# Performance work log

Measured on AMD Instinct MI355X. Metric: run time of the kernel, lower is better.

The kernel has to match this reference:

```python
import jax, jax.numpy as jnp
import numpy as np

N_NODES = 50000
N_EDGES = 800000
IN_CH, HID_CH, OUT_CH = 128, 128, 64


def setup_inputs() -> dict:
    key = jax.random.key(0)
    k1, k2, k3, k4, k5, k6 = jax.random.split(key, 6)
    x = jax.random.normal(k1, (N_NODES, IN_CH), dtype=jnp.float32)
    edge_index = jax.random.randint(k2, (2, N_EDGES), 0, N_NODES, dtype=jnp.int64)
    # nn.Linear params: W [out, in], b [out]
    W1 = jax.random.normal(k3, (HID_CH, IN_CH), dtype=jnp.float32) / np.sqrt(IN_CH)
    b1 = jax.random.normal(k4, (HID_CH,), dtype=jnp.float32) * 0.01
    W2 = jax.random.normal(k5, (OUT_CH, HID_CH), dtype=jnp.float32) / np.sqrt(HID_CH)
    b2 = jax.random.normal(k6, (OUT_CH,), dtype=jnp.float32) * 0.01
    return {"x": x, "edge_index": edge_index, "W1": W1, "b1": b1, "W2": W2, "b2": b2}


def _aggregate(x, edge_index):
    # Faithful to SimpleGNN.aggregate: deg from ROW counts, normalization gathered at DST (col).
    row, col = edge_index[0], edge_index[1]
    n = x.shape[0]
    deg = jnp.bincount(row, length=n).astype(x.dtype)
    deg_inv = jnp.where(deg > 0, 1.0 / deg, 0.0)
    # out[dst] += x[src] * deg_inv[dst]  ==  segment_sum(x[src] by dst) * deg_inv[dst]
    agg = jax.ops.segment_sum(x[row], col, num_segments=n)
    return agg * deg_inv[:, None]


def reference(x, edge_index, W1, b1, W2, b2):
    h = x @ W1.T + b1                 # [N, hidden]
    h = _aggregate(h, edge_index)     # degree-normalized scatter-add
    out = h @ W2.T + b2               # [N, out]
    return out
```

## Files before the change

### kernel.cpp

```cpp
#include <hip/hip_runtime.h>
#include <hip/hip_bf16.h>


#define IN_CH   128
#define OUT_CH  64
#define NCHUNK  64
#define NRANGE  8
#define RBINS   6272
#define NRANGE_H 4
#define RBINS_H 12544
#define MC_PAD  40
#define YROWS   32
#define PLACE_BLOCKS (NCHUNK * NRANGE)
#define SMEM_FLOATS (IN_CH * OUT_CH + YROWS * (IN_CH + 4))

typedef unsigned short u16;
typedef unsigned int u32;

static __device__ inline float bfu32_lo(u32 u) { return __uint_as_float(u << 16); }
static __device__ inline float bfu32_hi(u32 u) { return __uint_as_float(u & 0xffff0000u); }
static __device__ inline u16 f2bf(float f) {
    __hip_bfloat16 h = __float2bfloat16(f);
    return *reinterpret_cast<u16*>(&h);
}

static __device__ inline int detect_stride_wave(const int* __restrict__ ei) {
    int lane = threadIdx.x & 63;
    int idx = (lane < 32) ? (2 * lane + 1) : 1;
    int v = ei[idx];
    unsigned long long m = __ballot((v != 0) && (lane < 32));
    return (m == 0ull) ? 2 : 1;
}

static __device__ inline void y_unit(int t, const float* __restrict__ x,
                                     const float* __restrict__ M,
                                     u16* __restrict__ y, float* smem,
                                     int n_nodes) {
    int tid = threadIdx.x;
    float* Ms = smem;
    float (*xs)[IN_CH + 4] = (float(*)[IN_CH + 4])(smem + IN_CH * OUT_CH);
    int tx = tid & 15;
    int ty = tid >> 4;
    int row0 = t * YROWS;
    if (row0 >= n_nodes) return;

    const float4* Mv = (const float4*)M;
    float4* Msv = (float4*)Ms;
#pragma unroll
    for (int k = 0; k < 8; ++k) Msv[tid + 256 * k] = Mv[tid + 256 * k];

    for (int f = tid; f < YROWS * 32; f += 256) {
        int r = f >> 5, kq = f & 31;
        float4 v = make_float4(0.f, 0.f, 0.f, 0.f);
        if (row0 + r < n_nodes)
            v = *(const float4*)&x[(size_t)(row0 + r) * IN_CH + 4 * kq];
        *(float4*)&xs[r][4 * kq] = v;
    }
    __syncthreads();

    float4 acc0 = make_float4(0.f, 0.f, 0.f, 0.f);
    float4 acc1 = make_float4(0.f, 0.f, 0.f, 0.f);

    for (int k = 0; k < IN_CH; k += 4) {
        float4 xr0 = *(const float4*)&xs[ty][k];
        float4 xr1 = *(const float4*)&xs[ty + 16][k];
        float4 m0 = *(const float4*)&Ms[(k + 0) * OUT_CH + 4 * tx];
        float4 m1 = *(const float4*)&Ms[(k + 1) * OUT_CH + 4 * tx];
        float4 m2 = *(const float4*)&Ms[(k + 2) * OUT_CH + 4 * tx];
        float4 m3 = *(const float4*)&Ms[(k + 3) * OUT_CH + 4 * tx];
        acc0.x = fmaf(xr0.x, m0.x, acc0.x); acc0.y = fmaf(xr0.x, m0.y, acc0.y);
        acc0.z = fmaf(xr0.x, m0.z, acc0.z); acc0.w = fmaf(xr0.x, m0.w, acc0.w);
        acc0.x = fmaf(xr0.y, m1.x, acc0.x); acc0.y = fmaf(xr0.y, m1.y, acc0.y);
        acc0.z = fmaf(xr0.y, m1.z, acc0.z); acc0.w = fmaf(xr0.y, m1.w, acc0.w);
        acc0.x = fmaf(xr0.z, m2.x, acc0.x); acc0.y = fmaf(xr0.z, m2.y, acc0.y);
        acc0.z = fmaf(xr0.z, m2.z, acc0.z); acc0.w = fmaf(xr0.z, m2.w, acc0.w);
        acc0.x = fmaf(xr0.w, m3.x, acc0.x); acc0.y = fmaf(xr0.w, m3.y, acc0.y);
        acc0.z = fmaf(xr0.w, m3.z, acc0.z); acc0.w = fmaf(xr0.w, m3.w, acc0.w);
        acc1.x = fmaf(xr1.x, m0.x, acc1.x); acc1.y = fmaf(xr1.x, m0.y, acc1.y);
        acc1.z = fmaf(xr1.x, m0.z, acc1.z); acc1.w = fmaf(xr1.x, m0.w, acc1.w);
        acc1.x = fmaf(xr1.y, m1.x, acc1.x); acc1.y = fmaf(xr1.y, m1.y, acc1.y);
        acc1.z = fmaf(xr1.y, m1.z, acc1.z); acc1.w = fmaf(xr1.y, m1.w, acc1.w);
        acc1.x = fmaf(xr1.z, m2.x, acc1.x); acc1.y = fmaf(xr1.z, m2.y, acc1.y);
        acc1.z = fmaf(xr1.z, m2.z, acc1.z); acc1.w = fmaf(xr1.z, m2.w, acc1.w);
        acc1.x = fmaf(xr1.w, m3.x, acc1.x); acc1.y = fmaf(xr1.w, m3.y, acc1.y);
        acc1.z = fmaf(xr1.w, m3.z, acc1.z); acc1.w = fmaf(xr1.w, m3.w, acc1.w);
    }

    int r0 = row0 + ty;
    int r1 = row0 + ty + 16;
    if (r0 < n_nodes) {
        ushort4 s4;
        s4.x = f2bf(acc0.x); s4.y = f2bf(acc0.y);
        s4.z = f2bf(acc0.z); s4.w = f2bf(acc0.w);
        *(ushort4*)&y[(size_t)r0 * OUT_CH + 4 * tx] = s4;
    }
    if (r1 < n_nodes) {
        ushort4 s4;
        s4.x = f2bf(acc1.x); s4.y = f2bf(acc1.y);
        s4.z = f2bf(acc1.z); s4.w = f2bf(acc1.w);
        *(ushort4*)&y[(size_t)r1 * OUT_CH + 4 * tx] = s4;
    }
}

__global__ __launch_bounds__(256) void mk_prep(const float* __restrict__ W1,
                                               const float* __restrict__ b1,
                                               const float* __restrict__ W2,
                                               const int* __restrict__ ei,
                                               float* __restrict__ M,
                                               float* __restrict__ c,
                                               u16* __restrict__ row_slab,
                                               u16* __restrict__ col_slab,
                                               int* __restrict__ counter,
                                               int n_edges, int n_nodes) {
    __shared__ u32 bins[RBINS_H];
    int b = blockIdx.x;
    int tid = threadIdx.x;
    if (b < MC_PAD) {
        if (b == 0 && tid == 0) *counter = 0;
        int t = b * 256 + tid;
        if (t < IN_CH * OUT_CH) {
            int o = t & (OUT_CH - 1);
            int i = t >> 6;
            float acc = 0.f;
            for (int h = 0; h < 128; ++h)
                acc += W1[h * 128 + i] * W2[o * 128 + h];
            M[i * OUT_CH + o] = acc;
        } else if (t < IN_CH * OUT_CH + OUT_CH) {
            int o = t - IN_CH * OUT_CH;
            float acc = 0.f;
            for (int h = 0; h < 128; ++h)
                acc += b1[h] * W2[o * 128 + h];
            c[o] = acc;
        }
        return;
    }
    int hb = b - MC_PAD;
    int range = hb & (NRANGE_H - 1);
    int chunk = hb >> 2;

    int range_size = (n_nodes + NRANGE_H - 1) / NRANGE_H;
    int lo = range * range_size;
    int hi = lo + range_size; if (hi > n_nodes) hi = n_nodes;
    int nbins = hi - lo;
    if (nbins <= 0) return;

    int stride = detect_stride_wave(ei);
    for (int i = tid; i < nbins; i += 256) bins[i] = 0u;
    __syncthreads();

    size_t e0 = (size_t)chunk * n_edges / NCHUNK;
    size_t e1 = (size_t)(chunk + 1) * n_edges / NCHUNK;
    size_t cnt = e1 - e0;
    const int* rp = ei;
    const int* cp = ei + (size_t)n_edges * stride;

    size_t i = tid;
    int s[8], d[8];
    for (; i + 1792 < cnt; i += 2048) {
#pragma unroll
        for (int k = 0; k < 8; ++k) s[k] = rp[(e0 + i + 256 * k) * stride];
#pragma unroll
        for (int k = 0; k < 8; ++k) d[k] = cp[(e0 + i + 256 * k) * stride];
#pragma unroll
        for (int k = 0; k < 8; ++k) {
            if (s[k] >= lo && s[k] < hi) atomicAdd(&bins[s[k] - lo], 1u);
            if (d[k] >= lo && d[k] < hi && (unsigned)s[k] < (unsigned)n_nodes)
                atomicAdd(&bins[d[k] - lo], 0x10000u);
        }
    }
    for (; i < cnt; i += 256) {
        int ss = rp[(e0 + i) * stride];
        int dd = cp[(e0 + i) * stride];
        if (ss >= lo && ss < hi) atomicAdd(&bins[ss - lo], 1u);
        if (dd >= lo && dd < hi && (unsigned)ss < (unsigned)n_nodes)
            atomicAdd(&bins[dd - lo], 0x10000u);
    }
    __syncthreads();

    size_t base = (size_t)chunk * n_nodes + lo;
    for (int k = tid; k < nbins; k += 256) {
        u32 v = bins[k];
        row_slab[base + k] = (u16)(v & 0xFFFFu);
        col_slab[base + k] = (u16)(v >> 16);
    }
}

__global__ __launch_bounds__(256) void mk_choff_y(u16* __restrict__ row_slab,
                                                  u16* __restrict__ col_slab,
                                                  int* __restrict__ deg_row,
                                                  int* __restrict__ cnt_col,
                                                  int* __restrict__ cursor_part,
                                                  int* __restrict__ bsums,
                                                  int* __restrict__ counter,
                                                  int* __restrict__ bscan_g,
                                                  const float* __restrict__ x,
                                                  const float* __restrict__ M,
                                                  u16* __restrict__ y,
                                                  int n_nodes, int nb) {
    __shared__ float smem[SMEM_FLOATS];
    __shared__ int islast;
    int b = blockIdx.x;
    int t = threadIdx.x;

    if (b >= nb) {
        y_unit(b - nb, x, M, y, smem, n_nodes);
        return;
    }

    int* sm = (int*)smem;
    int n = b * 256 + t;
    int run = 0;
    if (n < n_nodes) {
        int sum = 0;
#pragma unroll 8
        for (int ch = 0; ch < NCHUNK; ++ch)
            sum += row_slab[(size_t)ch * n_nodes + n];
        deg_row[n] = sum;
#pragma unroll 8
        for (int ch = 0; ch < NCHUNK; ++ch) {
            int v = col_slab[(size_t)ch * n_nodes + n];
            col_slab[(size_t)ch * n_nodes + n] = (u16)run;
            run += v;
        }
        cnt_col[n] = run;
    }
    sm[t] = run;
    __syncthreads();
    for (int d = 1; d < 256; d <<= 1) {
        int add = (t >= d) ? sm[t - d] : 0;
        __syncthreads();
        sm[t] += add;
        __syncthreads();
    }
    if (n < n_nodes) cursor_part[n] = sm[t] - run;
    if (t == 255) bsums[b] = sm[t];

    __syncthreads();
    if (t == 0) {
        __threadfence();
        int old = atomicAdd(counter, 1);
        islast = (old == nb - 1);
    }
    __syncthreads();
    if (islast) {
        int v = (t < nb) ? atomicAdd(&bsums[t], 0) : 0;
        sm[t] = v;
        __syncthreads();
        for (int d = 1; d < 256; d <<= 1) {
            int add = (t >= d) ? sm[t - d] : 0;
            __syncthreads();
            sm[t] += add;
            __syncthreads();
        }
        bscan_g[t] = sm[t] - v;
    }
}

__global__ __launch_bounds__(256) void mk_place_y(const int* __restrict__ ei,
                                                  const int* __restrict__ cursor_part,
                                                  const int* __restrict__ bscan_g,
                                                  const u16* __restrict__ col_slab,
                                                  int* __restrict__ csr_src,
                                                  const float* __restrict__ x,
                                                  const float* __restrict__ M,
                                                  u16* __restrict__ y,
                                                  int n_edges, int n_nodes,
                                                  int y_split) {
    __shared__ float smem[SMEM_FLOATS];
    int b = blockIdx.x;
    int tid = threadIdx.x;

    if (b < PLACE_BLOCKS) {
        int* rank = (int*)smem;
        int* bscanL = (int*)smem + RBINS;

        int range = b & (NRANGE - 1);
        int chunk = b >> 3;
        int range_size = (n_nodes + NRANGE - 1) / NRANGE;
        int lo = range * range_size;
        int hi = lo + range_size; if (hi > n_nodes) hi = n_nodes;
        if (hi <= lo) return;

        int stride = detect_stride_wave(ei);
        bscanL[tid] = bscan_g[tid];
        for (int i = tid; i < hi - lo; i += 256) rank[i] = 0;
        __syncthreads();

        size_t e0 = (size_t)chunk * n_edges / NCHUNK;
        size_t e1 = (size_t)(chunk + 1) * n_edges / NCHUNK;
        size_t cnt = e1 - e0;
        const int* rp = ei;
        const int* cp = ei + (size_t)n_edges * stride;
        size_t slab_base = (size_t)chunk * n_nodes;

        size_t i = tid;
        int s[8], d[8], cpart[8], coff[8];
        for (; i + 1792 < cnt; i += 2048) {
#pragma unroll
            for (int k = 0; k < 8; ++k) s[k] = rp[(e0 + i + 256 * k) * stride];
#pragma unroll
            for (int k = 0; k < 8; ++k) d[k] = cp[(e0 + i + 256 * k) * stride];
#pragma unroll
            for (int k = 0; k < 8; ++k) {
                int dc = (d[k] >= lo && d[k] < hi) ? d[k] : lo;
                cpart[k] = cursor_part[dc];
                coff[k]  = (int)col_slab[slab_base + dc];
            }
#pragma unroll
            for (int k = 0; k < 8; ++k) {
                if (d[k] >= lo && d[k] < hi && (unsigned)s[k] < (unsigned)n_nodes) {
                    int r = atomicAdd(&rank[d[k] - lo], 1);
                    csr_src[cpart[k] + bscanL[d[k] >> 8] + coff[k] + r] = s[k];
                }
            }
        }
        for (; i < cnt; i += 256) {
            int ss = rp[(e0 + i) * stride];
            int dd = cp[(e0 + i) * stride];
            if (dd >= lo && dd < hi && (unsigned)ss < (unsigned)n_nodes) {
                int r = atomicAdd(&rank[dd - lo], 1);
                csr_src[cursor_part[dd] + bscanL[dd >> 8] + (int)col_slab[slab_base + dd] + r] = ss;
            }
        }
        return;
    }

    y_unit(y_split + (b - PLACE_BLOCKS), x, M, y, smem, n_nodes);
}

__global__ __launch_bounds__(256) void mk_agg_final(const int* __restrict__ cursor_part,
                                                    const int* __restrict__ bscan_g,
                                                    const int* __restrict__ cnt_col,
                                                    const int* __restrict__ csr_src,
                                                    const int* __restrict__ deg_row,
                                                    const uint2* __restrict__ yv,
                                                    const float* __restrict__ c,
                                                    const float* __restrict__ b2,
                                                    float* __restrict__ out,
                                                    int n_nodes) {
    int wave = threadIdx.x >> 6;
    int lane = threadIdx.x & 63;
    int dsub = lane >> 4;
    int ch   = lane & 15;
    int d = blockIdx.x * 16 + wave * 4 + dsub;
    if (d >= n_nodes) return;

    int start = cursor_part[d] + bscan_g[d >> 8];
    int cnt = cnt_col[d];
    int end = start + cnt;
    int e1m = end - 1;
    float a0 = 0.f, a1 = 0.f, a2 = 0.f, a3 = 0.f;
    for (int j = start; j < end; j += 8) {
        int idx[8], srcs[8];
#pragma unroll
        for (int k = 0; k < 8; ++k) {
            int t = j + k;
            idx[k] = t > e1m ? e1m : t;
        }
#pragma unroll
        for (int k = 0; k < 8; ++k) srcs[k] = csr_src[idx[k]];
        uint2 u[8];
#pragma unroll
        for (int k = 0; k < 8; ++k) u[k] = yv[(size_t)srcs[k] * 16 + ch];
#pragma unroll
        for (int k = 1; k < 8; ++k)
            if (j + k >= end) { u[k].x = 0u; u[k].y = 0u; }
#pragma unroll
        for (int k = 0; k < 8; ++k) {
            a0 += bfu32_lo(u[k].x);
            a1 += bfu32_hi(u[k].x);
            a2 += bfu32_lo(u[k].y);
            a3 += bfu32_hi(u[k].y);
        }
    }
    int dr = deg_row[d];
    float di = (dr > 0) ? (1.0f / (float)dr) : 0.f;
    float fc = di * (float)cnt;
    float4 cv = ((const float4*)c)[ch];
    float4 bv = ((const float4*)b2)[ch];
    float4 o;
    o.x = di * a0 + fc * cv.x + bv.x;
    o.y = di * a1 + fc * cv.y + bv.y;
    o.z = di * a2 + fc * cv.z + bv.z;
    o.w = di * a3 + fc * cv.w + bv.w;
    ((float4*)(out + (size_t)d * OUT_CH))[ch] = o;
}

extern "C" void kernel_launch(void* const* d_in, const int* in_sizes, int n_in,
                              void* d_out, int out_size, void* d_ws, size_t ws_size,
                              hipStream_t stream) {
    const float* x  = (const float*)d_in[0];
    const int*   ei = (const int*)d_in[1];
    const float* W1 = (const float*)d_in[2];
    const float* b1 = (const float*)d_in[3];
    const float* W2 = (const float*)d_in[4];
    const float* b2 = (const float*)d_in[5];
    float* out = (float*)d_out;

    const int n_nodes = in_sizes[0] / IN_CH;
    const int n_edges = in_sizes[1] / 2;

    const size_t slab_bytes = (((size_t)NCHUNK * n_nodes * 2) + 127) & ~(size_t)127;
    const size_t csr_bytes  = ((size_t)n_edges * 4 + 127) & ~(size_t)127;

    char* ws = (char*)d_ws;
    float* M        = (float*)(ws);
    float* c        = (float*)(ws + 32768);
    int*   deg_row  = (int*)  (ws + 33152);
    int*   cnt_col  = (int*)  (ws + 233216);
    int*   cursor   = (int*)  (ws + 433280);
    int*   bsums    = (int*)  (ws + 633344);
    int*   bscan_g  = (int*)  (ws + 634368);
    int*   counter  = (int*)  (ws + 635392);
    u16*   row_slab = (u16*)  (ws + 635520);
    u16*   col_slab = (u16*)  (ws + 635520 + slab_bytes);
    int*   csr_src  = (int*)  (ws + 635520 + 2 * slab_bytes);
    u16*   y        = (u16*)  (ws + 635520 + 2 * slab_bytes + csr_bytes);

    const int y_total = (n_nodes + YROWS - 1) / YROWS;
    const int nb = (n_nodes + 255) / 256;
    int y_split = 512 - nb;
    if (y_split > y_total) y_split = y_total;

    mk_prep<<<MC_PAD + NCHUNK * NRANGE_H, 256, 0, stream>>>(
        W1, b1, W2, ei, M, c, row_slab, col_slab, counter, n_edges, n_nodes);

    mk_choff_y<<<nb + y_split, 256, 0, stream>>>(
        row_slab, col_slab, deg_row, cnt_col, cursor, bsums, counter, bscan_g,
        x, M, y, n_nodes, nb);

    mk_place_y<<<PLACE_BLOCKS + (y_total - y_split), 256, 0, stream>>>(
        ei, cursor, bscan_g, col_slab, csr_src, x, M, y, n_edges, n_nodes,
        y_split);

    mk_agg_final<<<(n_nodes + 15) / 16, 256, 0, stream>>>(
        cursor, bscan_g, cnt_col, csr_src, deg_row, (const uint2*)y, c, b2, out,
        n_nodes);
}
```

Before: 156.1 us.

## Record per-edge rank during histogram to make CSR placement atomic-free

The histogram pass now stores, for each edge, the per-chunk rank returned by the shared-memory atomic on its destination bin. The placement kernel reads that rank instead of redoing shared atomics over node ranges, so each edge is read once rather than once per range, and the work splits into 256 sub-chunk blocks. The y-projection work moves entirely into the placement kernel, the choff kernel shrinks to scan work only, and chunk/range block indexing is reordered. The cost is an extra u16 per edge written and read through global memory.

```diff
diff --git a/kernel.cpp b/kernel.cpp
--- a/kernel.cpp
+++ b/kernel.cpp
@@ -5,13 +5,11 @@
 #define IN_CH   128
 #define OUT_CH  64
 #define NCHUNK  64
-#define NRANGE  8
-#define RBINS   6272
 #define NRANGE_H 4
 #define RBINS_H 12544
 #define MC_PAD  40
 #define YROWS   32
-#define PLACE_BLOCKS (NCHUNK * NRANGE)
+#define PLACE_BLOCKS 256
 #define SMEM_FLOATS (IN_CH * OUT_CH + YROWS * (IN_CH + 4))
 
 typedef unsigned short u16;
@@ -110,6 +108,7 @@
                                                float* __restrict__ c,
                                                u16* __restrict__ row_slab,
                                                u16* __restrict__ col_slab,
+                                               u16* __restrict__ erank,
                                                int* __restrict__ counter,
                                                int n_edges, int n_nodes) {
     __shared__ u32 bins[RBINS_H];
@@ -135,8 +134,8 @@
         return;
     }
     int hb = b - MC_PAD;
-    int range = hb & (NRANGE_H - 1);
-    int chunk = hb >> 2;
+    int chunk = hb & (NCHUNK - 1);
+    int range = hb >> 6;
 
     int range_size = (n_nodes + NRANGE_H - 1) / NRANGE_H;
     int lo = range * range_size;
@@ -164,16 +163,20 @@
 #pragma unroll
         for (int k = 0; k < 8; ++k) {
             if (s[k] >= lo && s[k] < hi) atomicAdd(&bins[s[k] - lo], 1u);
-            if (d[k] >= lo && d[k] < hi && (unsigned)s[k] < (unsigned)n_nodes)
-                atomicAdd(&bins[d[k] - lo], 0x10000u);
+            if (d[k] >= lo && d[k] < hi && (unsigned)s[k] < (unsigned)n_nodes) {
+                u32 old = atomicAdd(&bins[d[k] - lo], 0x10000u);
+                erank[e0 + i + 256 * k] = (u16)(old >> 16);
+            }
         }
     }
     for (; i < cnt; i += 256) {
         int ss = rp[(e0 + i) * stride];
         int dd = cp[(e0 + i) * stride];
         if (ss >= lo && ss < hi) atomicAdd(&bins[ss - lo], 1u);
-        if (dd >= lo && dd < hi && (unsigned)ss < (unsigned)n_nodes)
-            atomicAdd(&bins[dd - lo], 0x10000u);
+        if (dd >= lo && dd < hi && (unsigned)ss < (unsigned)n_nodes) {
+            u32 old = atomicAdd(&bins[dd - lo], 0x10000u);
+            erank[e0 + i] = (u16)(old >> 16);
+        }
     }
     __syncthreads();
 
@@ -185,29 +188,19 @@
     }
 }
 
-__global__ __launch_bounds__(256) void mk_choff_y(u16* __restrict__ row_slab,
-                                                  u16* __restrict__ col_slab,
-                                                  int* __restrict__ deg_row,
-                                                  int* __restrict__ cnt_col,
-                                                  int* __restrict__ cursor_part,
-                                                  int* __restrict__ bsums,
-                                                  int* __restrict__ counter,
-                                                  int* __restrict__ bscan_g,
-                                                  const float* __restrict__ x,
-                                                  const float* __restrict__ M,
-                                                  u16* __restrict__ y,
-                                                  int n_nodes, int nb) {
-    __shared__ float smem[SMEM_FLOATS];
+__global__ __launch_bounds__(256) void mk_choff(u16* __restrict__ row_slab,
+                                                u16* __restrict__ col_slab,
+                                                int* __restrict__ deg_row,
+                                                int* __restrict__ cnt_col,
+                                                int* __restrict__ cursor_part,
+                                                int* __restrict__ bsums,
+                                                int* __restrict__ counter,
+                                                int* __restrict__ bscan_g,
+                                                int n_nodes, int nb) {
+    __shared__ int sm[256];
     __shared__ int islast;
     int b = blockIdx.x;
     int t = threadIdx.x;
-
-    if (b >= nb) {
-        y_unit(b - nb, x, M, y, smem, n_nodes);
-        return;
-    }
-
-    int* sm = (int*)smem;
     int n = b * 256 + t;
     int run = 0;
     if (n < n_nodes) {
@@ -260,72 +253,70 @@
                                                   const int* __restrict__ cursor_part,
                                                   const int* __restrict__ bscan_g,
                                                   const u16* __restrict__ col_slab,
+                                                  const u16* __restrict__ erank,
                                                   int* __restrict__ csr_src,
                                                   const float* __restrict__ x,
                                                   const float* __restrict__ M,
                                                   u16* __restrict__ y,
-                                                  int n_edges, int n_nodes,
-                                                  int y_split) {
+                                                  int n_edges, int n_nodes) {
     __shared__ float smem[SMEM_FLOATS];
     int b = blockIdx.x;
     int tid = threadIdx.x;
 
     if (b < PLACE_BLOCKS) {
-        int* rank = (int*)smem;
-        int* bscanL = (int*)smem + RBINS;
-
-        int range = b & (NRANGE - 1);
-        int chunk = b >> 3;
-        int range_size = (n_nodes + NRANGE - 1) / NRANGE;
-        int lo = range * range_size;
-        int hi = lo + range_size; if (hi > n_nodes) hi = n_nodes;
-        if (hi <= lo) return;
-
+        int* bscanL = (int*)smem;
+        bscanL[tid] = bscan_g[tid];
+        __syncthreads();
+
+        int chunk = b >> 2;
+        int sub = b & 3;
         int stride = detect_stride_wave(ei);
-        bscanL[tid] = bscan_g[tid];
-        for (int i = tid; i < hi - lo; i += 256) rank[i] = 0;
-        __syncthreads();
 
         size_t e0 = (size_t)chunk * n_edges / NCHUNK;
         size_t e1 = (size_t)(chunk + 1) * n_edges / NCHUNK;
         size_t cnt = e1 - e0;
+        size_t s0 = e0 + (size_t)sub * cnt / 4;
+        size_t s1 = e0 + (size_t)(sub + 1) * cnt / 4;
         const int* rp = ei;
         const int* cp = ei + (size_t)n_edges * stride;
         size_t slab_base = (size_t)chunk * n_nodes;
 
-        size_t i = tid;
-        int s[8], d[8], cpart[8], coff[8];
-        for (; i + 1792 < cnt; i += 2048) {
-#pragma unroll
-            for (int k = 0; k < 8; ++k) s[k] = rp[(e0 + i + 256 * k) * stride];
-#pragma unroll
-            for (int k = 0; k < 8; ++k) d[k] = cp[(e0 + i + 256 * k) * stride];
-#pragma unroll
-            for (int k = 0; k < 8; ++k) {
-                int dc = (d[k] >= lo && d[k] < hi) ? d[k] : lo;
+        size_t i = s0 + tid;
+        int s4[4], d4[4], cpart[4], coff[4];
+        u16 r4[4];
+        for (; i + 768 < s1; i += 1024) {
+#pragma unroll
+            for (int k = 0; k < 4; ++k) s4[k] = rp[(i + 256 * k) * stride];
+#pragma unroll
+            for (int k = 0; k < 4; ++k) d4[k] = cp[(i + 256 * k) * stride];
+#pragma unroll
+            for (int k = 0; k < 4; ++k) r4[k] = erank[i + 256 * k];
+#pragma unroll
+            for (int k = 0; k < 4; ++k) {
+                int dc = ((unsigned)d4[k] < (unsigned)n_nodes) ? d4[k] : 0;
                 cpart[k] = cursor_part[dc];
                 coff[k]  = (int)col_slab[slab_base + dc];
             }
 #pragma unroll
-            for (int k = 0; k < 8; ++k) {
-                if (d[k] >= lo && d[k] < hi && (unsigned)s[k] < (unsigned)n_nodes) {
-                    int r = atomicAdd(&rank[d[k] - lo], 1);
-                    csr_src[cpart[k] + bscanL[d[k] >> 8] + coff[k] + r] = s[k];
+            for (int k = 0; k < 4; ++k) {
+                if ((unsigned)d4[k] < (unsigned)n_nodes &&
+                    (unsigned)s4[k] < (unsigned)n_nodes) {
+                    csr_src[cpart[k] + bscanL[d4[k] >> 8] + coff[k] + (int)r4[k]] = s4[k];
                 }
             }
         }
-        for (; i < cnt; i += 256) {
-            int ss = rp[(e0 + i) * stride];
-            int dd = cp[(e0 + i) * stride];
-            if (dd >= lo && dd < hi && (unsigned)ss < (unsigned)n_nodes) {
-                int r = atomicAdd(&rank[dd - lo], 1);
-                csr_src[cursor_part[dd] + bscanL[dd >> 8] + (int)col_slab[slab_base + dd] + r] = ss;
+        for (; i < s1; i += 256) {
+            int ss = rp[i * stride];
+            int dd = cp[i * stride];
+            if ((unsigned)dd < (unsigned)n_nodes && (unsigned)ss < (unsigned)n_nodes) {
+                csr_src[cursor_part[dd] + bscanL[dd >> 8] +
+                        (int)col_slab[slab_base + dd] + (int)erank[i]] = ss;
             }
         }
         return;
     }
 
-    y_unit(y_split + (b - PLACE_BLOCKS), x, M, y, smem, n_nodes);
+    y_unit(b - PLACE_BLOCKS, x, M, y, smem, n_nodes);
 }
 
 __global__ __launch_bounds__(256) void mk_agg_final(const int* __restrict__ cursor_part,
@@ -402,6 +393,7 @@
 
     const size_t slab_bytes = (((size_t)NCHUNK * n_nodes * 2) + 127) & ~(size_t)127;
     const size_t csr_bytes  = ((size_t)n_edges * 4 + 127) & ~(size_t)127;
+    const size_t y_bytes    = ((size_t)n_nodes * OUT_CH * 2 + 127) & ~(size_t)127;
 
     char* ws = (char*)d_ws;
     float* M        = (float*)(ws);
@@ -416,22 +408,22 @@
     u16*   col_slab = (u16*)  (ws + 635520 + slab_bytes);
     int*   csr_src  = (int*)  (ws + 635520 + 2 * slab_bytes);
     u16*   y        = (u16*)  (ws + 635520 + 2 * slab_bytes + csr_bytes);
+    u16*   erank    = (u16*)  (ws + 635520 + 2 * slab_bytes + csr_bytes + y_bytes);
 
     const int y_total = (n_nodes + YROWS - 1) / YROWS;
     const int nb = (n_nodes + 255) / 256;
-    int y_split = 512 - nb;
-    if (y_split > y_total) y_split = y_total;
 
     mk_prep<<<MC_PAD + NCHUNK * NRANGE_H, 256, 0, stream>>>(
-        W1, b1, W2, ei, M, c, row_slab, col_slab, counter, n_edges, n_nodes);
-
-    mk_choff_y<<<nb + y_split, 256, 0, stream>>>(
-        row_slab, col_slab, deg_row, cnt_col, cursor, bsums, counter, bscan_g,
-        x, M, y, n_nodes, nb);
-
-    mk_place_y<<<PLACE_BLOCKS + (y_total - y_split), 256, 0, stream>>>(
-        ei, cursor, bscan_g, col_slab, csr_src, x, M, y, n_edges, n_nodes,
-        y_split);
+        W1, b1, W2, ei, M, c, row_slab, col_slab, erank, counter,
+        n_edges, n_nodes);
+
+    mk_choff<<<nb, 256, 0, stream>>>(row_slab, col_slab, deg_row, cnt_col,
+                                     cursor, bsums, counter, bscan_g,
+                                     n_nodes, nb);
+
+    mk_place_y<<<PLACE_BLOCKS + y_total, 256, 0, stream>>>(
+        ei, cursor, bscan_g, col_slab, erank, csr_src, x, M, y,
+        n_edges, n_nodes);
 
     mk_agg_final<<<(n_nodes + 15) / 16, 256, 0, stream>>>(
         cursor, bscan_g, cnt_col, csr_src, deg_row, (const uint2*)y, c, b2, out,
```

Result: no change. 158.4 us (+1.5%).

## Merge four launches into two persistent kernels with grid-wide spin barriers

Applied to the files above, without the earlier changes.

Replaces the four-kernel pipeline with a zeroing kernel plus two persistent kernels. Inside each, phases are separated by atomic-counter spin barriers and work is handed out through atomic ticket queues. Phase 1 fuses the weight premultiply, the histogram, and the column offset/scan. Phase 2 fuses CSR placement with the y GEMM units, then aggregation in a grid-stride loop. The goal is to cut launch gaps and tail idling between stages. The risk is that the spin barriers deadlock unless every block is co-resident, and the single launch caps occupancy.

```diff
diff --git a/kernel.cpp b/kernel.cpp
--- a/kernel.cpp
+++ b/kernel.cpp
@@ -9,10 +9,17 @@
 #define RBINS   6272
 #define NRANGE_H 4
 #define RBINS_H 12544
-#define MC_PAD  40
 #define YROWS   32
-#define PLACE_BLOCKS (NCHUNK * NRANGE)
+#define PLACE_UNITS (NCHUNK * NRANGE)
+#define K1_BLOCKS  (NCHUNK * NRANGE_H)
+#define K2_BLOCKS  512
 #define SMEM_FLOATS (IN_CH * OUT_CH + YROWS * (IN_CH + 4))
+
+#define C_HIST_DONE  0
+#define C_CHOFF_TK   1
+#define C_CHOFF_DONE 2
+#define C_TKA        3
+#define C_DONEA      4
 
 typedef unsigned short u16;
 typedef unsigned int u32;
@@ -30,6 +37,10 @@
     int v = ei[idx];
     unsigned long long m = __ballot((v != 0) && (lane < 32));
     return (m == 0ull) ? 2 : 1;
+}
+
+__global__ __launch_bounds__(64) void mk_zero(int* __restrict__ cnt) {
+    if (threadIdx.x < 32) cnt[threadIdx.x] = 0;
 }
 
 static __device__ inline void y_unit(int t, const float* __restrict__ x,
@@ -102,149 +113,133 @@
     }
 }
 
-__global__ __launch_bounds__(256) void mk_prep(const float* __restrict__ W1,
-                                               const float* __restrict__ b1,
-                                               const float* __restrict__ W2,
-                                               const int* __restrict__ ei,
-                                               float* __restrict__ M,
-                                               float* __restrict__ c,
-                                               u16* __restrict__ row_slab,
-                                               u16* __restrict__ col_slab,
-                                               int* __restrict__ counter,
-                                               int n_edges, int n_nodes) {
-    __shared__ u32 bins[RBINS_H];
+__global__ __launch_bounds__(256) void mk_phase1(const float* __restrict__ W1,
+                                                 const float* __restrict__ b1,
+                                                 const float* __restrict__ W2,
+                                                 const int* __restrict__ ei,
+                                                 float* __restrict__ M,
+                                                 float* __restrict__ c,
+                                                 u16* __restrict__ row_slab,
+                                                 u16* __restrict__ col_slab,
+                                                 int* __restrict__ deg_row,
+                                                 int* __restrict__ cnt_col,
+                                                 int* __restrict__ cursor_part,
+                                                 int* __restrict__ bsums,
+                                                 int* __restrict__ bscan_g,
+                                                 int* __restrict__ cnt,
+                                                 int n_edges, int n_nodes, int nb) {
+    __shared__ __align__(16) u32 bins[RBINS_H];
+    __shared__ int tk, lastf;
     int b = blockIdx.x;
     int tid = threadIdx.x;
-    if (b < MC_PAD) {
-        if (b == 0 && tid == 0) *counter = 0;
-        int t = b * 256 + tid;
-        if (t < IN_CH * OUT_CH) {
-            int o = t & (OUT_CH - 1);
-            int i = t >> 6;
-            float acc = 0.f;
-            for (int h = 0; h < 128; ++h)
-                acc += W1[h * 128 + i] * W2[o * 128 + h];
-            M[i * OUT_CH + o] = acc;
-        } else if (t < IN_CH * OUT_CH + OUT_CH) {
-            int o = t - IN_CH * OUT_CH;
-            float acc = 0.f;
-            for (int h = 0; h < 128; ++h)
-                acc += b1[h] * W2[o * 128 + h];
-            c[o] = acc;
-        }
-        return;
-    }
-    int hb = b - MC_PAD;
-    int range = hb & (NRANGE_H - 1);
-    int chunk = hb >> 2;
-
-    int range_size = (n_nodes + NRANGE_H - 1) / NRANGE_H;
-    int lo = range * range_size;
-    int hi = lo + range_size; if (hi > n_nodes) hi = n_nodes;
-    int nbins = hi - lo;
-    if (nbins <= 0) return;
-
-    int stride = detect_stride_wave(ei);
-    for (int i = tid; i < nbins; i += 256) bins[i] = 0u;
-    __syncthreads();
-
-    size_t e0 = (size_t)chunk * n_edges / NCHUNK;
-    size_t e1 = (size_t)(chunk + 1) * n_edges / NCHUNK;
-    size_t cnt = e1 - e0;
-    const int* rp = ei;
-    const int* cp = ei + (size_t)n_edges * stride;
-
-    size_t i = tid;
-    int s[8], d[8];
-    for (; i + 1792 < cnt; i += 2048) {
-#pragma unroll
-        for (int k = 0; k < 8; ++k) s[k] = rp[(e0 + i + 256 * k) * stride];
-#pragma unroll
-        for (int k = 0; k < 8; ++k) d[k] = cp[(e0 + i + 256 * k) * stride];
-#pragma unroll
-        for (int k = 0; k < 8; ++k) {
-            if (s[k] >= lo && s[k] < hi) atomicAdd(&bins[s[k] - lo], 1u);
-            if (d[k] >= lo && d[k] < hi && (unsigned)s[k] < (unsigned)n_nodes)
-                atomicAdd(&bins[d[k] - lo], 0x10000u);
-        }
-    }
-    for (; i < cnt; i += 256) {
-        int ss = rp[(e0 + i) * stride];
-        int dd = cp[(e0 + i) * stride];
-        if (ss >= lo && ss < hi) atomicAdd(&bins[ss - lo], 1u);
-        if (dd >= lo && dd < hi && (unsigned)ss < (unsigned)n_nodes)
-            atomicAdd(&bins[dd - lo], 0x10000u);
-    }
-    __syncthreads();
-
-    size_t base = (size_t)chunk * n_nodes + lo;
-    for (int k = tid; k < nbins; k += 256) {
-        u32 v = bins[k];
-        row_slab[base + k] = (u16)(v & 0xFFFFu);
-        col_slab[base + k] = (u16)(v >> 16);
-    }
-}
-
-__global__ __launch_bounds__(256) void mk_choff_y(u16* __restrict__ row_slab,
-                                                  u16* __restrict__ col_slab,
-                                                  int* __restrict__ deg_row,
-                                                  int* __restrict__ cnt_col,
-                                                  int* __restrict__ cursor_part,
-                                                  int* __restrict__ bsums,
-                                                  int* __restrict__ counter,
-                                                  int* __restrict__ bscan_g,
-                                                  const float* __restrict__ x,
-                                                  const float* __restrict__ M,
-                                                  u16* __restrict__ y,
-                                                  int n_nodes, int nb) {
-    __shared__ float smem[SMEM_FLOATS];
-    __shared__ int islast;
-    int b = blockIdx.x;
-    int t = threadIdx.x;
-
-    if (b >= nb) {
-        y_unit(b - nb, x, M, y, smem, n_nodes);
-        return;
-    }
-
-    int* sm = (int*)smem;
-    int n = b * 256 + t;
-    int run = 0;
-    if (n < n_nodes) {
-        int sum = 0;
+
+    {
+        int t = b * 33 + tid;
+        if (tid < 33 && t < IN_CH * OUT_CH + OUT_CH) {
+            if (t < IN_CH * OUT_CH) {
+                int o = t & (OUT_CH - 1);
+                int i = t >> 6;
+                float acc = 0.f;
 #pragma unroll 8
-        for (int ch = 0; ch < NCHUNK; ++ch)
-            sum += row_slab[(size_t)ch * n_nodes + n];
-        deg_row[n] = sum;
+                for (int h = 0; h < 128; ++h)
+                    acc += W1[h * 128 + i] * W2[o * 128 + h];
+                M[i * OUT_CH + o] = acc;
+            } else {
+                int o = t - IN_CH * OUT_CH;
+                float acc = 0.f;
 #pragma unroll 8
-        for (int ch = 0; ch < NCHUNK; ++ch) {
-            int v = col_slab[(size_t)ch * n_nodes + n];
-            col_slab[(size_t)ch * n_nodes + n] = (u16)run;
-            run += v;
-        }
-        cnt_col[n] = run;
-    }
-    sm[t] = run;
-    __syncthreads();
-    for (int d = 1; d < 256; d <<= 1) {
-        int add = (t >= d) ? sm[t - d] : 0;
-        __syncthreads();
-        sm[t] += add;
-        __syncthreads();
-    }
-    if (n < n_nodes) cursor_part[n] = sm[t] - run;
-    if (t == 255) bsums[b] = sm[t];
-
-    __syncthreads();
-    if (t == 0) {
+                for (int h = 0; h < 128; ++h)
+                    acc += b1[h] * W2[o * 128 + h];
+                c[o] = acc;
+            }
+        }
+    }
+
+    {
+        int range = b & (NRANGE_H - 1);
+        int chunk = b >> 2;
+        int range_size = (n_nodes + NRANGE_H - 1) / NRANGE_H;
+        int lo = range * range_size;
+        int hi = lo + range_size; if (hi > n_nodes) hi = n_nodes;
+        int nbins = hi - lo;
+        if (nbins > 0) {
+            int stride = detect_stride_wave(ei);
+            for (int i = tid; i < nbins; i += 256) bins[i] = 0u;
+            __syncthreads();
+
+            size_t e0 = (size_t)chunk * n_edges / NCHUNK;
+            size_t e1 = (size_t)(chunk + 1) * n_edges / NCHUNK;
+            size_t cnte = e1 - e0;
+            const int* rp = ei;
+            const int* cp = ei + (size_t)n_edges * stride;
+
+            size_t i = tid;
+            int s[8], d[8];
+            for (; i + 1792 < cnte; i += 2048) {
+#pragma unroll
+                for (int k = 0; k < 8; ++k) s[k] = rp[(e0 + i + 256 * k) * stride];
+#pragma unroll
+                for (int k = 0; k < 8; ++k) d[k] = cp[(e0 + i + 256 * k) * stride];
+#pragma unroll
+                for (int k = 0; k < 8; ++k) {
+                    if (s[k] >= lo && s[k] < hi) atomicAdd(&bins[s[k] - lo], 1u);
+                    if (d[k] >= lo && d[k] < hi && (unsigned)s[k] < (unsigned)n_nodes)
+                        atomicAdd(&bins[d[k] - lo], 0x10000u);
+                }
+            }
+            for (; i < cnte; i += 256) {
+                int ss = rp[(e0 + i) * stride];
+                int dd = cp[(e0 + i) * stride];
+                if (ss >= lo && ss < hi) atomicAdd(&bins[ss - lo], 1u);
+                if (dd >= lo && dd < hi && (unsigned)ss < (unsigned)n_nodes)
+                    atomicAdd(&bins[dd - lo], 0x10000u);
+            }
+            __syncthreads();
+
+            size_t base = (size_t)chunk * n_nodes + lo;
+            for (int k = tid; k < nbins; k += 256) {
+                u32 v = bins[k];
+                row_slab[base + k] = (u16)(v & 0xFFFFu);
+                col_slab[base + k] = (u16)(v >> 16);
+            }
+        }
+    }
+
+    __syncthreads();
+    if (tid == 0) {
         __threadfence();
-        int old = atomicAdd(counter, 1);
-        islast = (old == nb - 1);
-    }
-    __syncthreads();
-    if (islast) {
-        int v = (t < nb) ? atomicAdd(&bsums[t], 0) : 0;
-        sm[t] = v;
+        atomicAdd(&cnt[C_HIST_DONE], 1);
+        while (atomicAdd(&cnt[C_HIST_DONE], 0) < K1_BLOCKS)
+            __builtin_amdgcn_s_sleep(2);
+    }
+    __syncthreads();
+    __threadfence();
+
+    int* sm = (int*)bins;
+    for (;;) {
+        __syncthreads();
+        if (tid == 0) tk = atomicAdd(&cnt[C_CHOFF_TK], 1);
+        __syncthreads();
+        if (tk >= nb) break;
+        int cb = tk;
+        int t = tid;
+        int n = cb * 256 + t;
+        int run = 0;
+        if (n < n_nodes) {
+            int sum = 0;
+#pragma unroll 8
+            for (int ch = 0; ch < NCHUNK; ++ch)
+                sum += row_slab[(size_t)ch * n_nodes + n];
+            deg_row[n] = sum;
+#pragma unroll 8
+            for (int ch = 0; ch < NCHUNK; ++ch) {
+                int v = col_slab[(size_t)ch * n_nodes + n];
+                col_slab[(size_t)ch * n_nodes + n] = (u16)run;
+                run += v;
+            }
+            cnt_col[n] = run;
+        }
+        sm[t] = run;
         __syncthreads();
         for (int d = 1; d < 256; d <<= 1) {
             int add = (t >= d) ? sm[t - d] : 0;
@@ -252,138 +247,182 @@
             sm[t] += add;
             __syncthreads();
         }
-        bscan_g[t] = sm[t] - v;
-    }
-}
-
-__global__ __launch_bounds__(256) void mk_place_y(const int* __restrict__ ei,
-                                                  const int* __restrict__ cursor_part,
-                                                  const int* __restrict__ bscan_g,
-                                                  const u16* __restrict__ col_slab,
-                                                  int* __restrict__ csr_src,
-                                                  const float* __restrict__ x,
-                                                  const float* __restrict__ M,
-                                                  u16* __restrict__ y,
-                                                  int n_edges, int n_nodes,
-                                                  int y_split) {
-    __shared__ float smem[SMEM_FLOATS];
-    int b = blockIdx.x;
-    int tid = threadIdx.x;
-
-    if (b < PLACE_BLOCKS) {
-        int* rank = (int*)smem;
-        int* bscanL = (int*)smem + RBINS;
-
-        int range = b & (NRANGE - 1);
-        int chunk = b >> 3;
-        int range_size = (n_nodes + NRANGE - 1) / NRANGE;
-        int lo = range * range_size;
-        int hi = lo + range_size; if (hi > n_nodes) hi = n_nodes;
-        if (hi <= lo) return;
-
-        int stride = detect_stride_wave(ei);
-        bscanL[tid] = bscan_g[tid];
-        for (int i = tid; i < hi - lo; i += 256) rank[i] = 0;
-        __syncthreads();
-
-        size_t e0 = (size_t)chunk * n_edges / NCHUNK;
-        size_t e1 = (size_t)(chunk + 1) * n_edges / NCHUNK;
-        size_t cnt = e1 - e0;
-        const int* rp = ei;
-        const int* cp = ei + (size_t)n_edges * stride;
-        size_t slab_base = (size_t)chunk * n_nodes;
-
-        size_t i = tid;
-        int s[8], d[8], cpart[8], coff[8];
-        for (; i + 1792 < cnt; i += 2048) {
-#pragma unroll
-            for (int k = 0; k < 8; ++k) s[k] = rp[(e0 + i + 256 * k) * stride];
-#pragma unroll
-            for (int k = 0; k < 8; ++k) d[k] = cp[(e0 + i + 256 * k) * stride];
-#pragma unroll
-            for (int k = 0; k < 8; ++k) {
-                int dc = (d[k] >= lo && d[k] < hi) ? d[k] : lo;
-                cpart[k] = cursor_part[dc];
-                coff[k]  = (int)col_slab[slab_base + dc];
-            }
-#pragma unroll
-            for (int k = 0; k < 8; ++k) {
-                if (d[k] >= lo && d[k] < hi && (unsigned)s[k] < (unsigned)n_nodes) {
-                    int r = atomicAdd(&rank[d[k] - lo], 1);
-                    csr_src[cpart[k] + bscanL[d[k] >> 8] + coff[k] + r] = s[k];
-                }
-            }
-        }
-        for (; i < cnt; i += 256) {
-            int ss = rp[(e0 + i) * stride];
-            int dd = cp[(e0 + i) * stride];
-            if (dd >= lo && dd < hi && (unsigned)ss < (unsigned)n_nodes) {
-                int r = atomicAdd(&rank[dd - lo], 1);
-                csr_src[cursor_part[dd] + bscanL[dd >> 8] + (int)col_slab[slab_base + dd] + r] = ss;
-            }
-        }
-        return;
-    }
-
-    y_unit(y_split + (b - PLACE_BLOCKS), x, M, y, smem, n_nodes);
-}
-
-__global__ __launch_bounds__(256) void mk_agg_final(const int* __restrict__ cursor_part,
+        if (n < n_nodes) cursor_part[n] = sm[t] - run;
+        if (t == 255) bsums[cb] = sm[t];
+
+        __syncthreads();
+        if (t == 0) {
+            __threadfence();
+            int od = atomicAdd(&cnt[C_CHOFF_DONE], 1);
+            lastf = (od == nb - 1);
+        }
+        __syncthreads();
+        if (lastf) {
+            int v = (t < nb) ? atomicAdd(&bsums[t], 0) : 0;
+            sm[t] = v;
+            __syncthreads();
+            for (int d = 1; d < 256; d <<= 1) {
+                int add = (t >= d) ? sm[t - d] : 0;
+                __syncthreads();
+                sm[t] += add;
+                __syncthreads();
+            }
+            bscan_g[t] = sm[t] - v;
+        }
+    }
+}
+
+__global__ __launch_bounds__(256, 2) void mk_phase2(const int* __restrict__ ei,
+                                                    const int* __restrict__ cursor_part,
                                                     const int* __restrict__ bscan_g,
+                                                    const u16* __restrict__ col_slab,
+                                                    int* __restrict__ csr_src,
+                                                    const float* __restrict__ x,
+                                                    const float* __restrict__ M,
+                                                    u16* __restrict__ y,
                                                     const int* __restrict__ cnt_col,
-                                                    const int* __restrict__ csr_src,
                                                     const int* __restrict__ deg_row,
-                                                    const uint2* __restrict__ yv,
                                                     const float* __restrict__ c,
                                                     const float* __restrict__ b2,
                                                     float* __restrict__ out,
-                                                    int n_nodes) {
-    int wave = threadIdx.x >> 6;
-    int lane = threadIdx.x & 63;
+                                                    int* __restrict__ cnt,
+                                                    int n_edges, int n_nodes,
+                                                    int y_total) {
+    __shared__ float smem[SMEM_FLOATS];
+    __shared__ int tk;
+    int tid = threadIdx.x;
+    int totalA = PLACE_UNITS + y_total;
+    int myn = 0;
+
+    for (;;) {
+        __syncthreads();
+        if (tid == 0) tk = atomicAdd(&cnt[C_TKA], 1);
+        __syncthreads();
+        int u = tk;
+        if (u >= totalA) break;
+        if (u < PLACE_UNITS) {
+            int* rank = (int*)smem;
+            int* bscanL = (int*)smem + RBINS;
+
+            int range = u & (NRANGE - 1);
+            int chunk = u >> 3;
+            int range_size = (n_nodes + NRANGE - 1) / NRANGE;
+            int lo = range * range_size;
+            int hi = lo + range_size; if (hi > n_nodes) hi = n_nodes;
+            if (hi > lo) {
+                int stride = detect_stride_wave(ei);
+                bscanL[tid] = bscan_g[tid];
+                for (int i = tid; i < hi - lo; i += 256) rank[i] = 0;
+                __syncthreads();
+
+                size_t e0 = (size_t)chunk * n_edges / NCHUNK;
+                size_t e1 = (size_t)(chunk + 1) * n_edges / NCHUNK;
+                size_t cnte = e1 - e0;
+                const int* rp = ei;
+                const int* cp = ei + (size_t)n_edges * stride;
+                size_t slab_base = (size_t)chunk * n_nodes;
+
+                size_t i = tid;
+                int s[8], d[8], cpart[8], coff[8];
+                for (; i + 1792 < cnte; i += 2048) {
+#pragma unroll
+                    for (int k = 0; k < 8; ++k) s[k] = rp[(e0 + i + 256 * k) * stride];
+#pragma unroll
+                    for (int k = 0; k < 8; ++k) d[k] = cp[(e0 + i + 256 * k) * stride];
+#pragma unroll
+                    for (int k = 0; k < 8; ++k) {
+                        int dc = (d[k] >= lo && d[k] < hi) ? d[k] : lo;
+                        cpart[k] = cursor_part[dc];
+                        coff[k]  = (int)col_slab[slab_base + dc];
+                    }
+#pragma unroll
+                    for (int k = 0; k < 8; ++k) {
+                        if (d[k] >= lo && d[k] < hi && (unsigned)s[k] < (unsigned)n_nodes) {
+                            int r = atomicAdd(&rank[d[k] - lo], 1);
+                            csr_src[cpart[k] + bscanL[d[k] >> 8] + coff[k] + r] = s[k];
+                        }
+                    }
+                }
+                for (; i < cnte; i += 256) {
+                    int ss = rp[(e0 + i) * stride];
+                    int dd = cp[(e0 + i) * stride];
+                    if (dd >= lo && dd < hi && (unsigned)ss < (unsigned)n_nodes) {
+                        int r = atomicAdd(&rank[dd - lo], 1);
+                        csr_src[cursor_part[dd] + bscanL[dd >> 8] +
+                                (int)col_slab[slab_base + dd] + r] = ss;
+                    }
+                }
+            }
+        } else {
+            y_unit(u - PLACE_UNITS, x, M, y, smem, n_nodes);
+        }
+        ++myn;
+    }
+
+    __syncthreads();
+    if (tid == 0) {
+        __threadfence();
+        atomicAdd(&cnt[C_DONEA], myn);
+        while (atomicAdd(&cnt[C_DONEA], 0) < totalA)
+            __builtin_amdgcn_s_sleep(2);
+    }
+    __syncthreads();
+    __threadfence();
+
+    int* bscanL = (int*)smem;
+    bscanL[tid] = bscan_g[tid];
+    __syncthreads();
+
+    int totalB = (n_nodes + 15) / 16;
+    const uint2* yv = (const uint2*)y;
+    int wave = tid >> 6;
+    int lane = tid & 63;
     int dsub = lane >> 4;
     int ch   = lane & 15;
-    int d = blockIdx.x * 16 + wave * 4 + dsub;
-    if (d >= n_nodes) return;
-
-    int start = cursor_part[d] + bscan_g[d >> 8];
-    int cnt = cnt_col[d];
-    int end = start + cnt;
-    int e1m = end - 1;
-    float a0 = 0.f, a1 = 0.f, a2 = 0.f, a3 = 0.f;
-    for (int j = start; j < end; j += 8) {
-        int idx[8], srcs[8];
-#pragma unroll
-        for (int k = 0; k < 8; ++k) {
-            int t = j + k;
-            idx[k] = t > e1m ? e1m : t;
-        }
-#pragma unroll
-        for (int k = 0; k < 8; ++k) srcs[k] = csr_src[idx[k]];
-        uint2 u[8];
-#pragma unroll
-        for (int k = 0; k < 8; ++k) u[k] = yv[(size_t)srcs[k] * 16 + ch];
-#pragma unroll
-        for (int k = 1; k < 8; ++k)
-            if (j + k >= end) { u[k].x = 0u; u[k].y = 0u; }
-#pragma unroll
-        for (int k = 0; k < 8; ++k) {
-            a0 += bfu32_lo(u[k].x);
-            a1 += bfu32_hi(u[k].x);
-            a2 += bfu32_lo(u[k].y);
-            a3 += bfu32_hi(u[k].y);
-        }
-    }
-    int dr = deg_row[d];
-    float di = (dr > 0) ? (1.0f / (float)dr) : 0.f;
-    float fc = di * (float)cnt;
-    float4 cv = ((const float4*)c)[ch];
-    float4 bv = ((const float4*)b2)[ch];
-    float4 o;
-    o.x = di * a0 + fc * cv.x + bv.x;
-    o.y = di * a1 + fc * cv.y + bv.y;
-    o.z = di * a2 + fc * cv.z + bv.z;
-    o.w = di * a3 + fc * cv.w + bv.w;
-    ((float4*)(out + (size_t)d * OUT_CH))[ch] = o;
+    for (int u = blockIdx.x; u < totalB; u += K2_BLOCKS) {
+        int d = u * 16 + wave * 4 + dsub;
+        if (d >= n_nodes) continue;
+
+        int start = cursor_part[d] + bscanL[d >> 8];
+        int cc = cnt_col[d];
+        int end = start + cc;
+        int e1m = end - 1;
+        float a0 = 0.f, a1 = 0.f, a2 = 0.f, a3 = 0.f;
+        for (int j = start; j < end; j += 8) {
+            int idx[8], srcs[8];
+#pragma unroll
+            for (int k = 0; k < 8; ++k) {
+                int t = j + k;
+                idx[k] = t > e1m ? e1m : t;
+            }
+#pragma unroll
+            for (int k = 0; k < 8; ++k) srcs[k] = csr_src[idx[k]];
+            uint2 u8[8];
+#pragma unroll
+            for (int k = 0; k < 8; ++k) u8[k] = yv[(size_t)srcs[k] * 16 + ch];
+#pragma unroll
+            for (int k = 1; k < 8; ++k)
+                if (j + k >= end) { u8[k].x = 0u; u8[k].y = 0u; }
+#pragma unroll
+            for (int k = 0; k < 8; ++k) {
+                a0 += bfu32_lo(u8[k].x);
+                a1 += bfu32_hi(u8[k].x);
+                a2 += bfu32_lo(u8[k].y);
+                a3 += bfu32_hi(u8[k].y);
+            }
+        }
+        int dr = deg_row[d];
+        float di = (dr > 0) ? (1.0f / (float)dr) : 0.f;
+        float fc = di * (float)cc;
+        float4 cv = ((const float4*)c)[ch];
+        float4 bv = ((const float4*)b2)[ch];
+        float4 o;
+        o.x = di * a0 + fc * cv.x + bv.x;
+        o.y = di * a1 + fc * cv.y + bv.y;
+        o.z = di * a2 + fc * cv.z + bv.z;
+        o.w = di * a3 + fc * cv.w + bv.w;
+        ((float4*)(out + (size_t)d * OUT_CH))[ch] = o;
+    }
 }
 
 extern "C" void kernel_launch(void* const* d_in, const int* in_sizes, int n_in,
@@ -411,7 +450,7 @@
     int*   cursor   = (int*)  (ws + 433280);
     int*   bsums    = (int*)  (ws + 633344);
     int*   bscan_g  = (int*)  (ws + 634368);
-    int*   counter  = (int*)  (ws + 635392);
+    int*   counters = (int*)  (ws + 635392);
     u16*   row_slab = (u16*)  (ws + 635520);
     u16*   col_slab = (u16*)  (ws + 635520 + slab_bytes);
     int*   csr_src  = (int*)  (ws + 635520 + 2 * slab_bytes);
@@ -419,21 +458,14 @@
 
     const int y_total = (n_nodes + YROWS - 1) / YROWS;
     const int nb = (n_nodes + 255) / 256;
-    int y_split = 512 - nb;
-    if (y_split > y_total) y_split = y_total;
-
-    mk_prep<<<MC_PAD + NCHUNK * NRANGE_H, 256, 0, stream>>>(
-        W1, b1, W2, ei, M, c, row_slab, col_slab, counter, n_edges, n_nodes);
-
-    mk_choff_y<<<nb + y_split, 256, 0, stream>>>(
-        row_slab, col_slab, deg_row, cnt_col, cursor, bsums, counter, bscan_g,
-        x, M, y, n_nodes, nb);
-
-    mk_place_y<<<PLACE_BLOCKS + (y_total - y_split), 256, 0, stream>>>(
-        ei, cursor, bscan_g, col_slab, csr_src, x, M, y, n_edges, n_nodes,
-        y_split);
-
-    mk_agg_final<<<(n_nodes + 15) / 16, 256, 0, stream>>>(
-        cursor, bscan_g, cnt_col, csr_src, deg_row, (const uint2*)y, c, b2, out,
-        n_nodes);
-}
+
+    mk_zero<<<1, 64, 0, stream>>>(counters);
+
+    mk_phase1<<<K1_BLOCKS, 256, 0, stream>>>(
+        W1, b1, W2, ei, M, c, row_slab, col_slab, deg_row, cnt_col,
+        cursor, bsums, bscan_g, counters, n_edges, n_nodes, nb);
+
+    mk_phase2<<<K2_BLOCKS, 256, 0, stream>>>(
+        ei, cursor, bscan_g, col_slab, csr_src, x, M, y,
+        cnt_col, deg_row, c, b2, out, counters, n_edges, n_nodes, y_total);
+}
```

Measured after the change: 297.3 us. 90.4% more time.
